# Kernel optimization log

Hardware: AMD Instinct MI355X
Metric: run time of the kernel (lower is better)

## Reference

```python
import jax, jax.numpy as jnp
import numpy as np

KERNEL = 7  # median blur window size (odd)


def setup_inputs() -> dict:
    key = jax.random.key(0)
    # NCHW image batch, values in [0,1) like normalized images
    img = jax.random.uniform(key, (8, 3, 512, 512), dtype=jnp.float32)
    return {"img": img}


def _median_blur(img, k):
    # Matches kornia.filters.median_blur: zero padding ('same'), then median
    # over the k*k window. k*k is odd so the exact middle of the sorted
    # window equals torch.median's lower median.
    pad = k // 2
    b, c, h, w = img.shape
    x = jnp.pad(img, ((0, 0), (0, 0), (pad, pad), (pad, pad)))  # zero pad
    # unfold: [B, C, k*k, H, W] — same materialization as kornia's conv2d
    # with binary one-hot kernels. Loop is over the fixed k*k = 49 taps.
    patches = jnp.stack(
        [x[:, :, i:i + h, j:j + w] for i in range(k) for j in range(k)],
        axis=2,
    )
    mid = (k * k) // 2
    return jnp.sort(patches, axis=2)[:, :, mid]  # [B, C, H, W]


def reference(img):
    return _median_blur(img, KERNEL)
```

## Files before the change

kernel.cpp:

```cpp
#include <hip/hip_runtime.h>
#include <utility>

#define IMG_H 512
#define IMG_W 512

typedef _Float16 h2 __attribute__((ext_vector_type(2)));

__device__ __forceinline__ h2 h2min(h2 a, h2 b) { return __builtin_elementwise_min(a, b); }
__device__ __forceinline__ h2 h2max(h2 a, h2 b) { return __builtin_elementwise_max(a, b); }

struct Op { int kind, a, b; };
constexpr int NSLOT = 320;
constexpr int MAXOPS = 4096;
struct Prog { Op ops[MAXOPS]; int n; bool ok; };

constexpr int pow2ceil(int x) { int p = 1; while (p < x) p += p; return p; }

struct Builder {
    Op ops[MAXOPS] = {};
    int n = 0;
    bool pad[NSLOT] = {};
    bool init[NSLOT] = {};
    bool ok = true;

    constexpr void emit(int k, int a, int b) {
        if (n < MAXOPS) ops[n++] = Op{k, a, b}; else ok = false;
    }
    constexpr void load(int s, int c) { emit(2, s, c); pad[s] = false; init[s] = true; }
    constexpr void mov(int d, int s) {
        if (!init[s]) ok = false;
        emit(1, d, s); pad[d] = pad[s]; init[d] = true;
    }
    constexpr void mkpad(int s) { pad[s] = true; init[s] = true; }
    constexpr void ce_(int a, int b) {
        if (!init[a] || !init[b]) { ok = false; return; }
        if (pad[a] && pad[b]) return;
        if (!pad[a] && pad[b]) return;
        if (pad[a] && !pad[b]) {
            emit(1, a, b); pad[a] = false; pad[b] = true; return;
        }
        emit(0, a, b);
    }
    constexpr void sort_run(int base, int len) {
        for (int p = 1; p < len; p += p)
            for (int k = p; k > 0; k /= 2)
                for (int j = k % p; j + k < len; j += k + k)
                    for (int i = 0; i < k; ++i)
                        if (i + j + k < len)
                            if ((i + j) / (p + p) == (i + j + k) / (p + p))
                                ce_(base + i + j, base + i + j + k);
    }
    constexpr void merge_stage(int base, int P) {
        int nn = 2 * P, p = P;
        for (int k = p; k > 0; k /= 2)
            for (int j = k % p; j + k < nn; j += k + k)
                for (int i = 0; i < k; ++i) {
                    int a = i + j, b = i + j + k;
                    if (b < nn && a / (p + p) == b / (p + p)) ce_(base + a, base + b);
                }
    }
    constexpr void load_col(int base, int c) {
        for (int r = 0; r < 7; ++r) load(base + r, c * 7 + r);
        sort_run(base, 7);
    }
    constexpr void place(int dst, int src, int len, int P) {
        for (int i = 0; i < len; ++i) mov(dst + i, src + i);
        for (int i = len; i < P; ++i) mkpad(dst + i);
    }
    constexpr void merge_to(int dst, int s1, int l1, int s2, int l2) {
        int P = pow2ceil(l1 > l2 ? l1 : l2);
        place(dst, s1, l1, P);
        place(dst + P, s2, l2, P);
        merge_stage(dst, P);
    }
    constexpr void outop(int o, int slot) {
        if (!init[slot] || pad[slot]) ok = false;
        emit(3, o, slot);
    }
};

constexpr Prog build() {
    Builder b{};
    constexpr int F34 = 0, F56 = 32, FC = 64, FP12 = 128, FP78 = 160;
    constexpr int C0 = 192, C9 = 200, C2c = 208, C7c = 216, FT = 224, FF = 256;

    b.load_col(F34, 3); b.mkpad(F34 + 7); b.load_col(F34 + 8, 4); b.mkpad(F34 + 15);
    b.merge_stage(F34, 8);
    b.load_col(F56, 5); b.mkpad(F56 + 7); b.load_col(F56 + 8, 6); b.mkpad(F56 + 15);
    b.merge_stage(F56, 8);
    b.merge_to(FC, F34, 14, F56, 14);

    b.load_col(FP12, 1); b.mkpad(FP12 + 7);
    b.load_col(FP12 + 8, 2);
    for (int i = 0; i < 7; ++i) b.mov(C2c + i, FP12 + 8 + i);
    b.mkpad(FP12 + 15); b.merge_stage(FP12, 8);

    b.load_col(FP78, 7);
    for (int i = 0; i < 7; ++i) b.mov(C7c + i, FP78 + i);
    b.mkpad(FP78 + 7); b.load_col(FP78 + 8, 8); b.mkpad(FP78 + 15);
    b.merge_stage(FP78, 8);

    b.load_col(C0, 0); b.load_col(C9, 9);

    b.merge_to(FT, FP12, 14, C0, 7);  b.merge_to(FF, FC, 28, FT, 21); b.outop(0, FF + 24);
    b.merge_to(FT, FP12, 14, C7c, 7); b.merge_to(FF, FC, 28, FT, 21); b.outop(1, FF + 24);
    b.merge_to(FT, FP78, 14, C2c, 7); b.merge_to(FF, FC, 28, FT, 21); b.outop(2, FF + 24);
    b.merge_to(FT, FP78, 14, C9, 7);  b.merge_to(FF, FC, 28, FT, 21); b.outop(3, FF + 24);

    Prog p{};
    bool needed[NSLOT] = {};
    int kindr[MAXOPS] = {};
    bool keep[MAXOPS] = {};
    for (int t = b.n - 1; t >= 0; --t) {
        Op o = b.ops[t];
        if (o.kind == 3) { keep[t] = true; kindr[t] = 3; needed[o.b] = true; }
        else if (o.kind == 0) {
            bool na = needed[o.a], nb = needed[o.b];
            if (na && nb)      { keep[t] = true; kindr[t] = 0; }
            else if (na)       { keep[t] = true; kindr[t] = 4; needed[o.b] = true; }
            else if (nb)       { keep[t] = true; kindr[t] = 5; needed[o.a] = true; }
        } else if (o.kind == 1) {
            if (needed[o.a]) { keep[t] = true; kindr[t] = 1; needed[o.a] = false; needed[o.b] = true; }
        } else if (o.kind == 2) {
            if (needed[o.a]) { keep[t] = true; kindr[t] = 2; needed[o.a] = false; }
        }
    }
    p.n = 0;
    for (int t = 0; t < b.n; ++t)
        if (keep[t]) { p.ops[p.n] = b.ops[t]; p.ops[p.n].kind = kindr[t]; ++p.n; }
    p.ok = b.ok;
    return p;
}

constexpr Prog PROG = build();
static_assert(PROG.ok && PROG.n > 0 && PROG.n < MAXOPS, "program build failed");

template <int I>
__device__ __forceinline__ void step(h2* v, const h2* cols, h2* med) {
    constexpr Op o = PROG.ops[I];
    if constexpr (o.kind == 0) {
        h2 lo = h2min(v[o.a], v[o.b]);
        h2 hi = h2max(v[o.a], v[o.b]);
        v[o.a] = lo; v[o.b] = hi;
    } else if constexpr (o.kind == 1) v[o.a] = v[o.b];
    else if constexpr (o.kind == 2) v[o.a] = cols[o.b];
    else if constexpr (o.kind == 3) med[o.a] = v[o.b];
    else if constexpr (o.kind == 4) v[o.a] = h2min(v[o.a], v[o.b]);
    else v[o.b] = h2max(v[o.a], v[o.b]);
}

template <size_t... Is>
__device__ __forceinline__ void run_all(h2* v, const h2* cols, h2* med,
                                        std::index_sequence<Is...>) {
    (step<(int)Is>(v, cols, med), ...);
}

__global__ __launch_bounds__(256) void median7x7_kernel(
        const float* __restrict__ img, float* __restrict__ out) {
    const int bc = blockIdx.z;
    const int tx = threadIdx.x;
    const int ty = threadIdx.y;
    const int x0 = (blockIdx.x * 64 + tx) * 4;
    const int y  = (blockIdx.y * 4 + ty) * 2;

    const float* base = img + (size_t)bc * (IMG_H * IMG_W);
    const bool okl = (x0 >= 4);
    const bool okr = (x0 <= 504);
    const int xl = okl ? (x0 - 4) : 0;
    const int xr = okr ? (x0 + 4) : 504;

    h2 colv[70];
    float prv[10];
#pragma unroll
    for (int r = 0; r < 8; ++r) {
        const int yy = y - 3 + r;
        float4 L, M, R;
        if ((unsigned)yy < IMG_H) {
            const float* rp = base + (size_t)yy * IMG_W;
            L = *(const float4*)(rp + xl);
            M = *(const float4*)(rp + x0);
            R = *(const float4*)(rp + xr);
        } else {
            L = make_float4(0.f, 0.f, 0.f, 0.f); M = L; R = L;
        }
        float cur[10];
        cur[0] = okl ? L.y : 0.f; cur[1] = okl ? L.z : 0.f; cur[2] = okl ? L.w : 0.f;
        cur[3] = M.x; cur[4] = M.y; cur[5] = M.z; cur[6] = M.w;
        cur[7] = okr ? R.x : 0.f; cur[8] = okr ? R.y : 0.f; cur[9] = okr ? R.z : 0.f;
        if (r > 0) {
#pragma unroll
            for (int c = 0; c < 10; ++c)
                colv[c * 7 + (r - 1)] = (h2)__builtin_amdgcn_cvt_pkrtz(prv[c], cur[c]);
        }
#pragma unroll
        for (int c = 0; c < 10; ++c) prv[c] = cur[c];
    }

    h2 v[NSLOT];
    h2 med[4];
    run_all(v, colv, med, std::make_index_sequence<(size_t)PROG.n>{});

    float* op = out + (size_t)bc * (IMG_H * IMG_W) + (size_t)y * IMG_W + x0;
    *(float4*)op = make_float4((float)med[0].x, (float)med[1].x,
                               (float)med[2].x, (float)med[3].x);
    *(float4*)(op + IMG_W) = make_float4((float)med[0].y, (float)med[1].y,
                                         (float)med[2].y, (float)med[3].y);
}

extern "C" void kernel_launch(void* const* d_in, const int* in_sizes, int n_in,
                              void* d_out, int out_size, void* d_ws, size_t ws_size,
                              hipStream_t stream) {
    const float* img = (const float*)d_in[0];
    float* out = (float*)d_out;
    dim3 grid(2, 64, 24);
    dim3 block(64, 4, 1);
    hipLaunchKernelGGL(median7x7_kernel, grid, block, 0, stream, img, out);
}
```

Measured before the change: 98.66 us.

## Replace full 49-element merges with a shared 42-element merge and median selection

Instead of merging a 28-element core with 21 other elements for each of four outputs, the program now builds a shared sorted 42-element set (core plus one column pair) and picks each output's median by combining it with a single sorted column. The selection uses a max of reversed-paired elements followed by a min-tree, which avoids two full 49-wide merge networks per output. The dead-code pruner is extended to handle the new min-only and max-only ops. This cuts min/max operation count but relies on the correctness of the rank-selection identity and may change register pressure.

```diff
diff --git a/kernel.cpp b/kernel.cpp
--- a/kernel.cpp
+++ b/kernel.cpp
@@ -40,6 +40,14 @@
             emit(1, a, b); pad[a] = false; pad[b] = true; return;
         }
         emit(0, a, b);
+    }
+    constexpr void maxin(int a, int b) {
+        if (!init[a] || !init[b] || pad[a] || pad[b]) ok = false;
+        emit(5, a, b);
+    }
+    constexpr void minin(int a, int b) {
+        if (!init[a] || !init[b] || pad[a] || pad[b]) ok = false;
+        emit(4, a, b);
     }
     constexpr void sort_run(int base, int len) {
         for (int p = 1; p < len; p += p)
@@ -73,39 +81,42 @@
         place(dst + P, s2, l2, P);
         merge_stage(dst, P);
     }
-    constexpr void outop(int o, int slot) {
-        if (!init[slot] || pad[slot]) ok = false;
-        emit(3, o, slot);
+    constexpr void select_med49(int T, int A, int B, int o) {
+        for (int t = 0; t < 7; ++t) {
+            mov(T + t, A + 17 + t);
+            maxin(B + 6 - t, T + t);
+        }
+        mov(T + 7, A + 24);
+        minin(T, T + 1); minin(T + 2, T + 3);
+        minin(T + 4, T + 5); minin(T + 6, T + 7);
+        minin(T, T + 2); minin(T + 4, T + 6);
+        minin(T, T + 4);
+        if (!init[T] || pad[T]) ok = false;
+        emit(3, o, T);
     }
 };
 
 constexpr Prog build() {
     Builder b{};
-    constexpr int F34 = 0, F56 = 32, FC = 64, FP12 = 128, FP78 = 160;
-    constexpr int C0 = 192, C9 = 200, C2c = 208, C7c = 216, FT = 224, FF = 256;
-
-    b.load_col(F34, 3); b.mkpad(F34 + 7); b.load_col(F34 + 8, 4); b.mkpad(F34 + 15);
-    b.merge_stage(F34, 8);
-    b.load_col(F56, 5); b.mkpad(F56 + 7); b.load_col(F56 + 8, 6); b.mkpad(F56 + 15);
-    b.merge_stage(F56, 8);
+    constexpr int F34 = 80, F56 = 112, FC = 144, FP12 = 176, FP78 = 208;
+    constexpr int C42 = 240;
+    constexpr int T0 = 304, T1 = 312;
+
+    for (int c = 0; c < 10; ++c) b.load_col(8 * c, c);
+
+    b.merge_to(F34, 8 * 3, 7, 8 * 4, 7);
+    b.merge_to(F56, 8 * 5, 7, 8 * 6, 7);
     b.merge_to(FC, F34, 14, F56, 14);
 
-    b.load_col(FP12, 1); b.mkpad(FP12 + 7);
-    b.load_col(FP12 + 8, 2);
-    for (int i = 0; i < 7; ++i) b.mov(C2c + i, FP12 + 8 + i);
-    b.mkpad(FP12 + 15); b.merge_stage(FP12, 8);
-
-    b.load_col(FP78, 7);
-    for (int i = 0; i < 7; ++i) b.mov(C7c + i, FP78 + i);
-    b.mkpad(FP78 + 7); b.load_col(FP78 + 8, 8); b.mkpad(FP78 + 15);
-    b.merge_stage(FP78, 8);
-
-    b.load_col(C0, 0); b.load_col(C9, 9);
-
-    b.merge_to(FT, FP12, 14, C0, 7);  b.merge_to(FF, FC, 28, FT, 21); b.outop(0, FF + 24);
-    b.merge_to(FT, FP12, 14, C7c, 7); b.merge_to(FF, FC, 28, FT, 21); b.outop(1, FF + 24);
-    b.merge_to(FT, FP78, 14, C2c, 7); b.merge_to(FF, FC, 28, FT, 21); b.outop(2, FF + 24);
-    b.merge_to(FT, FP78, 14, C9, 7);  b.merge_to(FF, FC, 28, FT, 21); b.outop(3, FF + 24);
+    b.merge_to(FP12, 8 * 1, 7, 8 * 2, 7);
+    b.merge_to(C42, FC, 28, FP12, 14);
+    b.select_med49(T0, C42, 8 * 0, 0);
+    b.select_med49(T1, C42, 8 * 7, 1);
+
+    b.merge_to(FP78, 8 * 7, 7, 8 * 8, 7);
+    b.merge_to(C42, FC, 28, FP78, 14);
+    b.select_med49(T0, C42, 8 * 2, 2);
+    b.select_med49(T1, C42, 8 * 9, 3);
 
     Prog p{};
     bool needed[NSLOT] = {};
@@ -123,6 +134,10 @@
             if (needed[o.a]) { keep[t] = true; kindr[t] = 1; needed[o.a] = false; needed[o.b] = true; }
         } else if (o.kind == 2) {
             if (needed[o.a]) { keep[t] = true; kindr[t] = 2; needed[o.a] = false; }
+        } else if (o.kind == 4) {
+            if (needed[o.a]) { keep[t] = true; kindr[t] = 4; needed[o.b] = true; }
+        } else if (o.kind == 5) {
+            if (needed[o.b]) { keep[t] = true; kindr[t] = 5; needed[o.a] = true; }
         }
     }
     p.n = 0;
```

Result: faster. 94.12 us (-4.6%).
